# Performance work log

Measured on AMD Instinct MI355X. Metric: run time of the kernel, lower is better.

The kernel has to match this reference:

```python
import jax, jax.numpy as jnp
import numpy as np

# ---- dims (see shape_source) ----
N_NODES = 100_000
N_EDGES = 600_000
N_GRAPHS = 512
N_NODE_FEAT = 90   # atom-type vocabulary
H = 128            # n_hidden_feat
E_FEAT = 256       # n_edge_net_feat
G_FEAT = 128       # n_graph_feat
N_CONV = 3         # n_conv * n_edge_labels, conv_labels = [0,0,0]
SCALE = 0.05


def setup_inputs() -> dict:
    key = jax.random.key(0)
    ks = jax.random.split(key, 16)
    nodes = jax.random.randint(ks[0], (N_NODES,), 0, N_NODE_FEAT)
    edge_sources = jax.random.randint(ks[1], (N_EDGES,), 0, N_NODES)
    edge_targets = jax.random.randint(ks[2], (N_EDGES,), 0, N_NODES)
    graph_indices = jnp.sort(jax.random.randint(ks[3], (N_NODES,), 0, N_GRAPHS))
    node_counts = jnp.maximum(jnp.bincount(graph_indices, length=N_GRAPHS), 1).astype(jnp.float32)

    def rn(k, shape):
        return jax.random.normal(k, shape, jnp.float32) * SCALE

    return {
        "nodes": nodes,
        "edge_sources": edge_sources,
        "edge_targets": edge_targets,
        "graph_indices": graph_indices,
        "node_counts": node_counts,
        # learned parameters
        "embed": rn(ks[4], (N_NODE_FEAT, H)),           # NodeEmbedding table
        "Wg": rn(ks[5], (N_CONV, H, H)),                # gate linear per conv (bias=False)
        "We1": rn(ks[6], (N_CONV, H, E_FEAT)),          # EdgeNetwork layer 1 per conv
        "We2": rn(ks[7], (N_CONV, E_FEAT, H)),          # EdgeNetwork layer 2 per conv
        "Wp": rn(ks[8], (H, H)),                        # LinearPooling
        "Wfc1": rn(ks[9], (H, G_FEAT)), "bfc1": jnp.zeros((G_FEAT,), jnp.float32),
        "Wfc2": rn(ks[10], (G_FEAT, G_FEAT)), "bfc2": jnp.zeros((G_FEAT,), jnp.float32),
        "Wr": rn(ks[11], (G_FEAT, 1)), "br": jnp.zeros((1,), jnp.float32),
    }


def reference(nodes, edge_sources, edge_targets, graph_indices, node_counts,
              embed, Wg, We1, We2, Wp, Wfc1, bfc1, Wfc2, bfc2, Wr, br):
    sp = jax.nn.softplus
    # NodeEmbedding: atom-type lookup -> [N, H]
    x = embed[nodes]
    # Gated graph convolutions: gather -> edge MLP + gate -> scatter-add -> residual
    for i in range(N_CONV):
        z = x[edge_sources]                               # [E, H] gather
        e = sp(z @ We1[i]) @ We2[i]                       # EdgeNetwork (2 layers, no shortcut)
        m = jax.nn.sigmoid(z @ Wg[i]) * sp(e)             # gate * edge_activation(message)
        agg = jax.ops.segment_sum(m, edge_targets, num_segments=N_NODES)  # scatter-add
        x = x + sp(agg)                                   # node_activation + residual
    # LinearPooling (last conv only): per-graph mean of linear(x)
    y = jax.ops.segment_sum(x @ Wp, graph_indices, num_segments=N_GRAPHS) / node_counts[:, None]
    # GraphPooling with n_steps=1: activation only (no batch norm)
    g = sp(y)
    # FullConnection stack (n_fc=2)
    g = sp(g @ Wfc1 + bfc1)
    g = sp(g @ Wfc2 + bfc2)
    return g @ Wr + br
```

## Files before the change

kernel.cpp:

```cpp
#include <hip/hip_runtime.h>
#include <hip/hip_bf16.h>

typedef unsigned short u16;
typedef __attribute__((ext_vector_type(8))) short short8;
typedef __attribute__((ext_vector_type(4))) float f32x4;
typedef __attribute__((ext_vector_type(16))) float f32x16;
typedef __attribute__((ext_vector_type(2))) __bf16 bf16x2;

#define NNODES 100000
#define NEDGES 600000
#define NGRAPHS 512
#define HF 128
#define EF 256
#define GB 32
#define NTILES 3125
#define GRID_CONV 512

#define PLD 264
__device__ __forceinline__ int cidx(int chunk, int row){ return chunk * PLD + row * 8; }

__device__ __forceinline__ float bfu(u16 u){ return __uint_as_float(((unsigned)u) << 16); }
__device__ __forceinline__ u16 f2bf(float f){
    unsigned u = __float_as_uint(f);
    unsigned r = (u + 0x7fff + ((u >> 16) & 1)) >> 16;
    return (u16)r;
}
__device__ __forceinline__ unsigned pack2(float a, float b){
    bf16x2 v = { (__bf16)a, (__bf16)b };
    return __builtin_bit_cast(unsigned, v);
}

#if __has_builtin(__builtin_amdgcn_rcpf)
#define RCP1(x) __builtin_amdgcn_rcpf(x)
#else
#define RCP1(x) (1.f / (x))
#endif

__device__ __forceinline__ float sp_f(float x){
    return __logf(1.f + __expf(x));
}
__device__ __forceinline__ float sig_f(float x){
    return RCP1(1.f + __expf(-x));
}
__device__ __forceinline__ float lf(const void* p, long i, bool f32){
    return f32 ? ((const float*)p)[i] : bfu(((const u16*)p)[i]);
}

__device__ __forceinline__ bool is_f32(const void* probe){
    const u16* p = (const u16*)probe;
    int lane = threadIdx.x & 63;
    int c = 0;
#pragma unroll
    for (int i = 0; i < 4; i++) c += (fabsf(bfu(p[lane * 4 + i])) > 1.0f) ? 1 : 0;
#pragma unroll
    for (int off = 32; off; off >>= 1) c += __shfl_xor(c, off, 64);
    return c > 8;
}

__global__ __launch_bounds__(256) void prep_kernel(const void* __restrict__ wg,
                                                   const void* __restrict__ we1,
                                                   const void* __restrict__ we2,
                                                   const void* __restrict__ wp,
                                                   const void* __restrict__ wfc1,
                                                   const void* __restrict__ wfc2,
                                                   u16* __restrict__ pwg,
                                                   u16* __restrict__ pwe1,
                                                   u16* __restrict__ pwe2,
                                                   u16* __restrict__ pwp,
                                                   u16* __restrict__ pf1,
                                                   u16* __restrict__ pf2,
                                                   const void* __restrict__ emb,
                                                   const int* __restrict__ tgt,
                                                   int* __restrict__ counts,
                                                   float* __restrict__ xsum){
    int b = blockIdx.x, t = threadIdx.x;
    if (b < 960) {
        bool f32 = is_f32(emb);
        int i = b * 256 + t;
        int c = i / 81920, r = i % 81920;
        const void* src; u16* dst; int N, KN, l;
        if (r < 16384)      { src = wg;  dst = pwg;  N = HF; KN = 16384; l = r; }
        else if (r < 49152) { src = we1; dst = pwe1; N = EF; KN = 32768; l = r - 16384; }
        else                { src = we2; dst = pwe2; N = HF; KN = 32768; l = r - 49152; }
        int j = l & 7, lane = (l >> 3) & 63, rest = l >> 9;
        int NT = N >> 5;
        int nt = rest % NT, ks = rest / NT;
        int k = ks * 16 + (lane >> 5) * 8 + j;
        int n = nt * 32 + (lane & 31);
        long base = (long)c * KN;
        dst[base + l] = f2bf(lf(src, base + (long)k * N + n, f32));
    } else if (b < 1152) {
        bool f32 = is_f32(emb);
        int i = (b - 960) * 256 + t;
        int c = i / 16384, l = i % 16384;
        const void* src = (c == 0) ? wp : (c == 1) ? wfc1 : wfc2;
        u16* dst = (c == 0) ? pwp : (c == 1) ? pf1 : pf2;
        int j = l & 7, lane = (l >> 3) & 63, rest = l >> 9;
        int nt = rest & 7, kt = rest >> 3;
        int k = kt * 32 + (lane >> 4) * 8 + j;
        int n = nt * 16 + (lane & 15);
        dst[l] = f2bf(lf(src, (long)k * HF + n, f32));
    } else if (b < 3496) {
        int e = (b - 1152) * 256 + t;
        if (e < NEDGES) atomicAdd(&counts[tgt[e]], 1);
    } else {
        int i = (b - 3496) * 256 + t;
        ((float4*)xsum)[i] = make_float4(0.f, 0.f, 0.f, 0.f);
    }
}

__global__ __launch_bounds__(256) void scan1_kernel(const int* __restrict__ counts,
                                                    int* __restrict__ row_ptr,
                                                    int* __restrict__ bsums){
    __shared__ int s[256];
    int t = threadIdx.x;
    int i = blockIdx.x * 256 + t;
    int v = (i < NNODES) ? counts[i] : 0;
    s[t] = v; __syncthreads();
    for (int off = 1; off < 256; off <<= 1) {
        int a = (t >= off) ? s[t - off] : 0;
        __syncthreads();
        s[t] += a;
        __syncthreads();
    }
    if (i < NNODES) row_ptr[i] = s[t] - v;
    if (t == 255) bsums[blockIdx.x] = s[255];
}

__global__ __launch_bounds__(512) void scan2_kernel(const int* __restrict__ bsums,
                                                    int* __restrict__ boffs, int nb){
    __shared__ int s[512];
    int t = threadIdx.x;
    int v = (t < nb) ? bsums[t] : 0;
    s[t] = v; __syncthreads();
    for (int off = 1; off < 512; off <<= 1) {
        int a = (t >= off) ? s[t - off] : 0;
        __syncthreads();
        s[t] += a;
        __syncthreads();
    }
    if (t < nb) boffs[t] = s[t] - v;
}

__global__ __launch_bounds__(256) void scan3_kernel(int* __restrict__ row_ptr,
                                                    const int* __restrict__ boffs,
                                                    int* __restrict__ cursor){
    int i = blockIdx.x * 256 + threadIdx.x;
    if (i < NNODES) {
        int r = row_ptr[i] + boffs[blockIdx.x];
        row_ptr[i] = r;
        cursor[i]  = r;
    }
}

__global__ __launch_bounds__(256) void fill_kernel(const int* __restrict__ src,
                                                   const int* __restrict__ tgt,
                                                   int* __restrict__ cursor,
                                                   int* __restrict__ es){
    int e = blockIdx.x * 256 + threadIdx.x;
    if (e < NEDGES) {
        int pos = atomicAdd(&cursor[tgt[e]], 1);
        es[pos] = src[e];
    }
}

struct ConvW { short8 wu0[8], wu1[8], wc[16], wg[8]; };

__device__ __forceinline__ void load_w(ConvW& W, const u16* __restrict__ pwg,
                                       const u16* __restrict__ pwe1,
                                       const u16* __restrict__ pwe2,
                                       int w, int lane){
#pragma unroll
    for (int ks = 0; ks < 8; ks++) {
        W.wu0[ks] = *(const short8*)(pwe1 + (((ks * 8 + w) * 64 + lane) << 3));
        W.wu1[ks] = *(const short8*)(pwe1 + (((ks * 8 + w + 4) * 64 + lane) << 3));
        W.wg[ks]  = *(const short8*)(pwg  + (((ks * 4 + w) * 64 + lane) << 3));
    }
#pragma unroll
    for (int jj = 0; jj < 16; jj++)
        W.wc[jj] = *(const short8*)(pwe2 + (((jj * 4 + w) * 64 + lane) << 3));
}

__device__ __forceinline__ void conv_loop1(const ConvW& W, const u16* xs, u16* us,
                                           int w, int lane, f32x16& aG_out){
    const int half = lane >> 5, nn = lane & 31;
    f32x16 acc0 = {}, acc1 = {}, g = {};
#pragma unroll
    for (int ks = 0; ks < 8; ks++) {
        short8 B = *(const short8*)(&xs[cidx(ks * 2 + half, nn)]);
        acc0 = __builtin_amdgcn_mfma_f32_32x32x16_bf16(W.wu0[ks], B, acc0, 0, 0, 0);
        acc1 = __builtin_amdgcn_mfma_f32_32x32x16_bf16(W.wu1[ks], B, acc1, 0, 0, 0);
        g    = __builtin_amdgcn_mfma_f32_32x32x16_bf16(W.wg[ks],  B, g,    0, 0, 0);
    }
#pragma unroll
    for (int q = 0; q < 4; q++) {
        uint2 d;
        d.x = pack2(sp_f(acc0[q*4+0]), sp_f(acc0[q*4+1]));
        d.y = pack2(sp_f(acc0[q*4+2]), sp_f(acc0[q*4+3]));
        *(uint2*)(&us[cidx(w * 4 + q, nn) + half * 4]) = d;
        uint2 e;
        e.x = pack2(sp_f(acc1[q*4+0]), sp_f(acc1[q*4+1]));
        e.y = pack2(sp_f(acc1[q*4+2]), sp_f(acc1[q*4+3]));
        *(uint2*)(&us[cidx(16 + w * 4 + q, nn) + half * 4]) = e;
    }
    aG_out = g;
}

__device__ __forceinline__ void conv_loop2(const ConvW& W, const u16* us,
                                           const f32x16& aG, u16* __restrict__ M,
                                           long row0, int w, int lane){
    const int half = lane >> 5, nn = lane & 31;
    f32x16 aT = {};
#pragma unroll
    for (int jj = 0; jj < 16; jj++) {
        short8 B = *(const short8*)(&us[cidx(jj * 2 + half, nn)]);
        aT = __builtin_amdgcn_mfma_f32_32x32x16_bf16(W.wc[jj], B, aT, 0, 0, 0);
    }
    long node = row0 + nn;
#pragma unroll
    for (int q = 0; q < 4; q++) {
        int h0 = w * 32 + half * 4 + q * 8;
        uint2 d;
        d.x = pack2(sig_f(aG[q*4+0]) * sp_f(aT[q*4+0]),
                    sig_f(aG[q*4+1]) * sp_f(aT[q*4+1]));
        d.y = pack2(sig_f(aG[q*4+2]) * sp_f(aT[q*4+2]),
                    sig_f(aG[q*4+3]) * sp_f(aT[q*4+3]));
        *(uint2*)(M + node * HF + h0) = d;
    }
}

__global__ __launch_bounds__(256, 2) void conv0_mfma(const int* __restrict__ nodes,
                                                     const void* __restrict__ emb,
                                                     u16* __restrict__ x,
                                                     const u16* __restrict__ pwg,
                                                     const u16* __restrict__ pwe1,
                                                     const u16* __restrict__ pwe2,
                                                     u16* __restrict__ M){
    __shared__ u16 xs[16 * PLD];
    __shared__ u16 us[32 * PLD];
    const int t = threadIdx.x;
    const int w = t >> 6, lane = t & 63;
    const int r0 = t >> 4, q = t & 15;
    const bool f32 = is_f32(emb);

    ConvW W;
    load_w(W, pwg, pwe1, pwe2, w, lane);

    const float4* ef = (const float4*)emb;
    const uint4*  eu = (const uint4*)emb;
    uint4* xg = (uint4*)x;

    int tile = blockIdx.x;
    {
        long row0 = (long)tile * 32;
        int v0 = nodes[row0 + r0], v1 = nodes[row0 + r0 + 16];
        uint4 b0, b1;
        if (f32) {
            float4 f0 = ef[(long)v0 * 32 + q * 2], f1 = ef[(long)v0 * 32 + q * 2 + 1];
            float4 f2 = ef[(long)v1 * 32 + q * 2], f3 = ef[(long)v1 * 32 + q * 2 + 1];
            b0.x = pack2(f0.x, f0.y); b0.y = pack2(f0.z, f0.w);
            b0.z = pack2(f1.x, f1.y); b0.w = pack2(f1.z, f1.w);
            b1.x = pack2(f2.x, f2.y); b1.y = pack2(f2.z, f2.w);
            b1.z = pack2(f3.x, f3.y); b1.w = pack2(f3.z, f3.w);
        } else {
            b0 = eu[(long)v0 * 16 + q];
            b1 = eu[(long)v1 * 16 + q];
        }
        xg[(row0 + r0) * 16 + q] = b0;
        xg[(row0 + r0 + 16) * 16 + q] = b1;
        *(uint4*)(&xs[cidx(q, r0)]) = b0;
        *(uint4*)(&xs[cidx(q, r0 + 16)]) = b1;
    }
    __syncthreads();

    for (;;) {
        long row0 = (long)tile * 32;
        int nxt = tile + GRID_CONV;
        bool have = nxt < NTILES;
        uint4 nb0 = {}, nb1 = {};
        float4 nf0 = {}, nf1 = {}, nf2 = {}, nf3 = {};
        if (have) {
            long nr = (long)nxt * 32;
            int v0 = nodes[nr + r0], v1 = nodes[nr + r0 + 16];
            if (f32) {
                nf0 = ef[(long)v0 * 32 + q * 2]; nf1 = ef[(long)v0 * 32 + q * 2 + 1];
                nf2 = ef[(long)v1 * 32 + q * 2]; nf3 = ef[(long)v1 * 32 + q * 2 + 1];
            } else {
                nb0 = eu[(long)v0 * 16 + q];
                nb1 = eu[(long)v1 * 16 + q];
            }
        }
        f32x16 aG;
        conv_loop1(W, xs, us, w, lane, aG);
        __syncthreads();
        if (have) {
            uint4 b0 = nb0, b1 = nb1;
            if (f32) {
                b0.x = pack2(nf0.x, nf0.y); b0.y = pack2(nf0.z, nf0.w);
                b0.z = pack2(nf1.x, nf1.y); b0.w = pack2(nf1.z, nf1.w);
                b1.x = pack2(nf2.x, nf2.y); b1.y = pack2(nf2.z, nf2.w);
                b1.z = pack2(nf3.x, nf3.y); b1.w = pack2(nf3.z, nf3.w);
            }
            long nr = (long)nxt * 32;
            xg[(nr + r0) * 16 + q] = b0;
            xg[(nr + r0 + 16) * 16 + q] = b1;
            *(uint4*)(&xs[cidx(q, r0)]) = b0;
            *(uint4*)(&xs[cidx(q, r0 + 16)]) = b1;
        }
        conv_loop2(W, us, aG, M, row0, w, lane);
        if (!have) break;
        __syncthreads();
        tile = nxt;
    }
}

__global__ __launch_bounds__(256, 2) void conv_mfma(const u16* __restrict__ x,
                                                    const u16* __restrict__ pwg,
                                                    const u16* __restrict__ pwe1,
                                                    const u16* __restrict__ pwe2,
                                                    u16* __restrict__ M){
    __shared__ u16 xs[16 * PLD];
    __shared__ u16 us[32 * PLD];
    const int t = threadIdx.x;
    const int w = t >> 6, lane = t & 63;
    const int r0 = t >> 4, q = t & 15;

    ConvW W;
    load_w(W, pwg, pwe1, pwe2, w, lane);

    const uint4* xg = (const uint4*)x;
    int tile = blockIdx.x;
    {
        long row0 = (long)tile * 32;
        uint4 b0 = xg[(row0 + r0) * 16 + q];
        uint4 b1 = xg[(row0 + r0 + 16) * 16 + q];
        *(uint4*)(&xs[cidx(q, r0)]) = b0;
        *(uint4*)(&xs[cidx(q, r0 + 16)]) = b1;
    }
    __syncthreads();

    for (;;) {
        long row0 = (long)tile * 32;
        int nxt = tile + GRID_CONV;
        bool have = nxt < NTILES;
        uint4 nb0 = {}, nb1 = {};
        if (have) {
            long nr = (long)nxt * 32;
            nb0 = xg[(nr + r0) * 16 + q];
            nb1 = xg[(nr + r0 + 16) * 16 + q];
        }
        f32x16 aG;
        conv_loop1(W, xs, us, w, lane, aG);
        __syncthreads();
        if (have) {
            *(uint4*)(&xs[cidx(q, r0)]) = nb0;
            *(uint4*)(&xs[cidx(q, r0 + 16)]) = nb1;
        }
        conv_loop2(W, us, aG, M, row0, w, lane);
        if (!have) break;
        __syncthreads();
        tile = nxt;
    }
}

__global__ __launch_bounds__(256) void agg_kernel(const u16* __restrict__ M,
                                                  const int* __restrict__ row_ptr,
                                                  const int* __restrict__ counts,
                                                  const int* __restrict__ es,
                                                  u16* __restrict__ x){
    int wid = blockIdx.x * 4 + (threadIdx.x >> 6);
    int lane = threadIdx.x & 63;
    long v = (long)wid * 4 + (lane >> 4);
    int l = lane & 15;
    if (v >= NNODES) return;
    int start = row_ptr[v], cnt = counts[v];
    float a0=0.f,a1=0.f,a2=0.f,a3=0.f,a4=0.f,a5=0.f,a6=0.f,a7=0.f;
    float b0=0.f,b1=0.f,b2=0.f,b3=0.f,b4=0.f,b5=0.f,b6=0.f,b7=0.f;
    const uint4* Mu = (const uint4*)M;
    int e = 0;
    for (; e + 3 < cnt; e += 4) {
        int s0 = es[start + e],     s1 = es[start + e + 1];
        int s2 = es[start + e + 2], s3 = es[start + e + 3];
        uint4 u0 = Mu[(long)s0 * 16 + l];
        uint4 u1 = Mu[(long)s1 * 16 + l];
        uint4 u2 = Mu[(long)s2 * 16 + l];
        uint4 u3 = Mu[(long)s3 * 16 + l];
        a0 += bfu((u16)u0.x); a1 += bfu((u16)(u0.x >> 16));
        a2 += bfu((u16)u0.y); a3 += bfu((u16)(u0.y >> 16));
        a4 += bfu((u16)u0.z); a5 += bfu((u16)(u0.z >> 16));
        a6 += bfu((u16)u0.w); a7 += bfu((u16)(u0.w >> 16));
        b0 += bfu((u16)u1.x); b1 += bfu((u16)(u1.x >> 16));
        b2 += bfu((u16)u1.y); b3 += bfu((u16)(u1.y >> 16));
        b4 += bfu((u16)u1.z); b5 += bfu((u16)(u1.z >> 16));
        b6 += bfu((u16)u1.w); b7 += bfu((u16)(u1.w >> 16));
        a0 += bfu((u16)u2.x); a1 += bfu((u16)(u2.x >> 16));
        a2 += bfu((u16)u2.y); a3 += bfu((u16)(u2.y >> 16));
        a4 += bfu((u16)u2.z); a5 += bfu((u16)(u2.z >> 16));
        a6 += bfu((u16)u2.w); a7 += bfu((u16)(u2.w >> 16));
        b0 += bfu((u16)u3.x); b1 += bfu((u16)(u3.x >> 16));
        b2 += bfu((u16)u3.y); b3 += bfu((u16)(u3.y >> 16));
        b4 += bfu((u16)u3.z); b5 += bfu((u16)(u3.z >> 16));
        b6 += bfu((u16)u3.w); b7 += bfu((u16)(u3.w >> 16));
    }
    for (; e < cnt; e++) {
        int s0 = es[start + e];
        uint4 u0 = Mu[(long)s0 * 16 + l];
        a0 += bfu((u16)u0.x); a1 += bfu((u16)(u0.x >> 16));
        a2 += bfu((u16)u0.y); a3 += bfu((u16)(u0.y >> 16));
        a4 += bfu((u16)u0.z); a5 += bfu((u16)(u0.z >> 16));
        a6 += bfu((u16)u0.w); a7 += bfu((u16)(u0.w >> 16));
    }
    a0 += b0; a1 += b1; a2 += b2; a3 += b3;
    a4 += b4; a5 += b5; a6 += b6; a7 += b7;
    uint4* xu = (uint4*)x;
    uint4 xv = xu[v * 16 + l];
    xv.x = pack2(bfu((u16)xv.x) + sp_f(a0), bfu((u16)(xv.x >> 16)) + sp_f(a1));
    xv.y = pack2(bfu((u16)xv.y) + sp_f(a2), bfu((u16)(xv.y >> 16)) + sp_f(a3));
    xv.z = pack2(bfu((u16)xv.z) + sp_f(a4), bfu((u16)(xv.z >> 16)) + sp_f(a5));
    xv.w = pack2(bfu((u16)xv.w) + sp_f(a6), bfu((u16)(xv.w >> 16)) + sp_f(a7));
    xu[v * 16 + l] = xv;
}

__global__ __launch_bounds__(256) void pool_kernel(const u16* __restrict__ x,
                                                   const int* __restrict__ gidx,
                                                   float* __restrict__ xsum){
    int wave = blockIdx.x * 4 + (threadIdx.x >> 6);
    int lane = threadIdx.x & 63;
    long base = (long)wave * 64;
    if (base >= NNODES) return;
    long end = base + 64; if (end > NNODES) end = NNODES;
    const unsigned* xu = (const unsigned*)x;
    int gcur = gidx[base];
    float a0 = 0.f, a1 = 0.f;
    for (long v = base; v < end; v++) {
        int g = gidx[v];
        if (g != gcur) {
            atomicAdd(&xsum[gcur * HF + lane * 2 + 0], a0);
            atomicAdd(&xsum[gcur * HF + lane * 2 + 1], a1);
            a0 = a1 = 0.f; gcur = g;
        }
        unsigned u = xu[v * 64 + lane];
        a0 += bfu((u16)u);
        a1 += bfu((u16)(u >> 16));
    }
    atomicAdd(&xsum[gcur * HF + lane * 2 + 0], a0);
    atomicAdd(&xsum[gcur * HF + lane * 2 + 1], a1);
}

__global__ __launch_bounds__(256) void head_mfma(const float* __restrict__ xsum,
                                                 const void* __restrict__ ncnt,
                                                 const u16* __restrict__ pwp,
                                                 const u16* __restrict__ pf1,
                                                 const u16* __restrict__ pf2,
                                                 const void* __restrict__ bfc1,
                                                 const void* __restrict__ bfc2,
                                                 const void* __restrict__ Wr,
                                                 const void* __restrict__ br,
                                                 void* __restrict__ out,
                                                 const void* __restrict__ probe){
    __shared__ u16 hibuf[2][GB][136];
    __shared__ u16 lobuf[2][GB][136];
    const int t = threadIdx.x;
    const int w = t >> 6, lane = t & 63;
    const int quad = lane >> 4, nr = lane & 15;
    const bool f32 = is_f32(probe);
    const int g0 = blockIdx.x * GB;

    for (int i = t; i < GB * 64; i += 256) {
        int g = i >> 6, c = (i & 63) * 2;
        float f0 = xsum[(g0 + g) * HF + c], f1 = xsum[(g0 + g) * HF + c + 1];
        u16 h0 = f2bf(f0), h1 = f2bf(f1);
        *(unsigned*)&hibuf[0][g][c] = (unsigned)h0 | ((unsigned)h1 << 16);
        *(unsigned*)&lobuf[0][g][c] = pack2(f0 - bfu(h0), f1 - bfu(h1));
    }
    __syncthreads();

    float rc[2];
#pragma unroll
    for (int nt = 0; nt < 2; nt++) rc[nt] = RCP1(lf(ncnt, g0 + nt * 16 + nr, f32));

    int cur = 0;
    for (int layer = 0; layer < 3; layer++) {
        const u16* pw = (layer == 0) ? pwp : (layer == 1) ? pf1 : pf2;
        const void* bias = (layer == 1) ? bfc1 : bfc2;
        int nxt = cur ^ 1;
#pragma unroll
        for (int c = 0; c < 2; c++) {
            int et = w * 2 + c;
            short8 A[4];
#pragma unroll
            for (int kt = 0; kt < 4; kt++)
                A[kt] = *(const short8*)(pw + (((kt * 8 + et) * 64 + lane) << 3));
#pragma unroll
            for (int nt = 0; nt < 2; nt++) {
                f32x4 acc = {0.f, 0.f, 0.f, 0.f};
#pragma unroll
                for (int kt = 0; kt < 4; kt++) {
                    short8 bh = *(const short8*)(&hibuf[cur][nt * 16 + nr][kt * 32 + quad * 8]);
                    short8 bl = *(const short8*)(&lobuf[cur][nt * 16 + nr][kt * 32 + quad * 8]);
                    acc = __builtin_amdgcn_mfma_f32_16x16x32_bf16(A[kt], bh, acc, 0, 0, 0);
                    acc = __builtin_amdgcn_mfma_f32_16x16x32_bf16(A[kt], bl, acc, 0, 0, 0);
                }
                int feat0 = et * 16 + quad * 4;
                float f[4];
#pragma unroll
                for (int r = 0; r < 4; r++) {
                    float a = (layer == 0) ? acc[r] * rc[nt]
                                           : acc[r] + lf(bias, feat0 + r, f32);
                    f[r] = sp_f(a);
                }
                u16 h[4]; float lo[4];
#pragma unroll
                for (int r = 0; r < 4; r++) { h[r] = f2bf(f[r]); lo[r] = f[r] - bfu(h[r]); }
                uint2 dh, dl;
                dh.x = (unsigned)h[0] | ((unsigned)h[1] << 16);
                dh.y = (unsigned)h[2] | ((unsigned)h[3] << 16);
                dl.x = pack2(lo[0], lo[1]);
                dl.y = pack2(lo[2], lo[3]);
                *(uint2*)&hibuf[nxt][nt * 16 + nr][feat0] = dh;
                *(uint2*)&lobuf[nxt][nt * 16 + nr][feat0] = dl;
            }
        }
        __syncthreads();
        cur = nxt;
    }

    int g = t >> 3, sub = t & 7;
    float p = 0.f;
    for (int k = sub * 16; k < sub * 16 + 16; k++) {
        float v = bfu(hibuf[cur][g][k]) + bfu(lobuf[cur][g][k]);
        p += v * lf(Wr, k, f32);
    }
    p += __shfl_down(p, 4, 64);
    p += __shfl_down(p, 2, 64);
    p += __shfl_down(p, 1, 64);
    if (sub == 0) {
        float res = p + lf(br, 0, f32);
        if (f32) ((float*)out)[g0 + g] = res;
        else     ((u16*)out)[g0 + g]  = f2bf(res);
    }
}

extern "C" void kernel_launch(void* const* d_in, const int* in_sizes, int n_in,
                              void* d_out, int out_size, void* d_ws, size_t ws_size,
                              hipStream_t stream) {
    const int* nodes = (const int*)d_in[0];
    const int* esrc  = (const int*)d_in[1];
    const int* etgt  = (const int*)d_in[2];
    const int* gidx  = (const int*)d_in[3];

    size_t off = 0;
    char* w = (char*)d_ws;
    auto take = [&](size_t bytes) -> void* {
        void* p = w + off;
        off = (off + bytes + 255) & ~(size_t)255;
        return p;
    };

    u16* pwg     = (u16*)take((size_t)3 * HF * HF * 2);
    u16* pwe1    = (u16*)take((size_t)3 * HF * EF * 2);
    u16* pwe2    = (u16*)take((size_t)3 * EF * HF * 2);
    u16* pwp     = (u16*)take((size_t)HF * HF * 2);
    u16* pf1     = (u16*)take((size_t)HF * HF * 2);
    u16* pf2     = (u16*)take((size_t)HF * HF * 2);
    int* counts  = (int*)take((size_t)NNODES * 4);
    int* row_ptr = (int*)take((size_t)NNODES * 4);
    int* cursor  = (int*)take((size_t)NNODES * 4);
    int* es      = (int*)take((size_t)NEDGES * 4);
    int* bsums   = (int*)take(2048);
    int* boffs   = (int*)take(2048);
    float* xsum  = (float*)take((size_t)NGRAPHS * HF * 4);
    u16* x       = (u16*)take((size_t)NNODES * HF * 2);
    u16* M       = (u16*)take((size_t)NNODES * HF * 2);

    hipMemsetAsync(counts, 0, (size_t)NNODES * 4, stream);

    prep_kernel<<<3560, 256, 0, stream>>>(d_in[6], d_in[7], d_in[8],
                                          d_in[9], d_in[10], d_in[12],
                                          pwg, pwe1, pwe2, pwp, pf1, pf2,
                                          d_in[5], etgt, counts, xsum);

    const int NB_SCAN = (NNODES + 255) / 256;
    const int NB_EDGE = (NEDGES + 255) / 256;
    scan1_kernel<<<NB_SCAN, 256, 0, stream>>>(counts, row_ptr, bsums);
    scan2_kernel<<<1, 512, 0, stream>>>(bsums, boffs, NB_SCAN);
    scan3_kernel<<<NB_SCAN, 256, 0, stream>>>(row_ptr, boffs, cursor);
    fill_kernel<<<NB_EDGE, 256, 0, stream>>>(esrc, etgt, cursor, es);

    const int NBA = (NNODES + 15) / 16;
    conv0_mfma<<<GRID_CONV, 256, 0, stream>>>(nodes, d_in[5], x, pwg, pwe1, pwe2, M);
    agg_kernel<<<NBA, 256, 0, stream>>>(M, row_ptr, counts, es, x);
    conv_mfma<<<GRID_CONV, 256, 0, stream>>>(x,
        pwg + (size_t)1 * HF * HF, pwe1 + (size_t)1 * HF * EF, pwe2 + (size_t)1 * EF * HF, M);
    agg_kernel<<<NBA, 256, 0, stream>>>(M, row_ptr, counts, es, x);
    conv_mfma<<<GRID_CONV, 256, 0, stream>>>(x,
        pwg + (size_t)2 * HF * HF, pwe1 + (size_t)2 * HF * EF, pwe2 + (size_t)2 * EF * HF, M);
    agg_kernel<<<NBA, 256, 0, stream>>>(M, row_ptr, counts, es, x);

    pool_kernel<<<(NNODES + 255) / 256, 256, 0, stream>>>(x, gidx, xsum);
    head_mfma<<<NGRAPHS / GB, 256, 0, stream>>>(xsum, d_in[4], pwp, pf1, pf2,
                                                d_in[11], d_in[13], d_in[14], d_in[15],
                                                d_out, d_in[5]);
}
```

Measured before the change: 388.0 us.

## Stage edge-network weights in LDS instead of registers, halve conv grid

Moves the EdgeNetwork weight fragments (We1, We2) out of per-thread registers into a large dynamic LDS buffer (about 153 KB per block), and reads the gate weights directly from global memory in each tile. The conv grid drops from 512 to 256 blocks, since only one block per CU fits with that LDS footprint. The aim is to free VGPRs and avoid per-wave redundant weight registers. In exchange every MFMA now needs extra LDS and global loads, and occupancy is limited to one block per CU.

```diff
diff --git a/kernel.cpp b/kernel.cpp
--- a/kernel.cpp
+++ b/kernel.cpp
@@ -14,10 +14,12 @@
 #define EF 256
 #define GB 32
 #define NTILES 3125
-#define GRID_CONV 512
+#define CONV_GRID 256
 
 #define PLD 264
 __device__ __forceinline__ int cidx(int chunk, int row){ return chunk * PLD + row * 8; }
+
+#define SMEM_BYTES 156416
 
 __device__ __forceinline__ float bfu(u16 u){ return __uint_as_float(((unsigned)u) << 16); }
 __device__ __forceinline__ u16 f2bf(float f){
@@ -164,58 +166,57 @@
     }
 }
 
-struct ConvW { short8 wu0[8], wu1[8], wc[16], wg[8]; };
-
-__device__ __forceinline__ void load_w(ConvW& W, const u16* __restrict__ pwg,
-                                       const u16* __restrict__ pwe1,
-                                       const u16* __restrict__ pwe2,
-                                       int w, int lane){
-#pragma unroll
-    for (int ks = 0; ks < 8; ks++) {
-        W.wu0[ks] = *(const short8*)(pwe1 + (((ks * 8 + w) * 64 + lane) << 3));
-        W.wu1[ks] = *(const short8*)(pwe1 + (((ks * 8 + w + 4) * 64 + lane) << 3));
-        W.wg[ks]  = *(const short8*)(pwg  + (((ks * 4 + w) * 64 + lane) << 3));
-    }
-#pragma unroll
-    for (int jj = 0; jj < 16; jj++)
-        W.wc[jj] = *(const short8*)(pwe2 + (((jj * 4 + w) * 64 + lane) << 3));
-}
-
-__device__ __forceinline__ void conv_loop1(const ConvW& W, const u16* xs, u16* us,
-                                           int w, int lane, f32x16& aG_out){
+__device__ __forceinline__ void conv_tile(const u16* w1, const u16* w2,
+                                          const u16* xs, u16* us,
+                                          const u16* __restrict__ pwg,
+                                          f32x16& aG_out, f32x16& aT_out,
+                                          int w, int lane, int phase){
     const int half = lane >> 5, nn = lane & 31;
-    f32x16 acc0 = {}, acc1 = {}, g = {};
-#pragma unroll
-    for (int ks = 0; ks < 8; ks++) {
-        short8 B = *(const short8*)(&xs[cidx(ks * 2 + half, nn)]);
-        acc0 = __builtin_amdgcn_mfma_f32_32x32x16_bf16(W.wu0[ks], B, acc0, 0, 0, 0);
-        acc1 = __builtin_amdgcn_mfma_f32_32x32x16_bf16(W.wu1[ks], B, acc1, 0, 0, 0);
-        g    = __builtin_amdgcn_mfma_f32_32x32x16_bf16(W.wg[ks],  B, g,    0, 0, 0);
-    }
-#pragma unroll
-    for (int q = 0; q < 4; q++) {
-        uint2 d;
-        d.x = pack2(sp_f(acc0[q*4+0]), sp_f(acc0[q*4+1]));
-        d.y = pack2(sp_f(acc0[q*4+2]), sp_f(acc0[q*4+3]));
-        *(uint2*)(&us[cidx(w * 4 + q, nn) + half * 4]) = d;
-        uint2 e;
-        e.x = pack2(sp_f(acc1[q*4+0]), sp_f(acc1[q*4+1]));
-        e.y = pack2(sp_f(acc1[q*4+2]), sp_f(acc1[q*4+3]));
-        *(uint2*)(&us[cidx(16 + w * 4 + q, nn) + half * 4]) = e;
-    }
-    aG_out = g;
-}
-
-__device__ __forceinline__ void conv_loop2(const ConvW& W, const u16* us,
-                                           const f32x16& aG, u16* __restrict__ M,
-                                           long row0, int w, int lane){
+    if (phase == 0) {
+        f32x16 acc0 = {}, acc1 = {};
+#pragma unroll
+        for (int ks = 0; ks < 8; ks++) {
+            short8 A0 = *(const short8*)(w1 + (((ks * 8 + w) * 64 + lane) << 3));
+            short8 A1 = *(const short8*)(w1 + (((ks * 8 + w + 4) * 64 + lane) << 3));
+            short8 B  = *(const short8*)(&xs[cidx(ks * 2 + half, nn)]);
+            acc0 = __builtin_amdgcn_mfma_f32_32x32x16_bf16(A0, B, acc0, 0, 0, 0);
+            acc1 = __builtin_amdgcn_mfma_f32_32x32x16_bf16(A1, B, acc1, 0, 0, 0);
+        }
+#pragma unroll
+        for (int q = 0; q < 4; q++) {
+            uint2 d;
+            d.x = pack2(sp_f(acc0[q*4+0]), sp_f(acc0[q*4+1]));
+            d.y = pack2(sp_f(acc0[q*4+2]), sp_f(acc0[q*4+3]));
+            *(uint2*)(&us[cidx(w * 4 + q, nn) + half * 4]) = d;
+            uint2 e;
+            e.x = pack2(sp_f(acc1[q*4+0]), sp_f(acc1[q*4+1]));
+            e.y = pack2(sp_f(acc1[q*4+2]), sp_f(acc1[q*4+3]));
+            *(uint2*)(&us[cidx(16 + w * 4 + q, nn) + half * 4]) = e;
+        }
+        f32x16 aG = {};
+#pragma unroll
+        for (int ks = 0; ks < 8; ks++) {
+            short8 A = *(const short8*)(pwg + (((ks * 4 + w) * 64 + lane) << 3));
+            short8 B = *(const short8*)(&xs[cidx(ks * 2 + half, nn)]);
+            aG = __builtin_amdgcn_mfma_f32_32x32x16_bf16(A, B, aG, 0, 0, 0);
+        }
+        aG_out = aG;
+    } else {
+        f32x16 aT = {};
+#pragma unroll
+        for (int jj = 0; jj < 16; jj++) {
+            short8 A = *(const short8*)(w2 + (((jj * 4 + w) * 64 + lane) << 3));
+            short8 B = *(const short8*)(&us[cidx(jj * 2 + half, nn)]);
+            aT = __builtin_amdgcn_mfma_f32_32x32x16_bf16(A, B, aT, 0, 0, 0);
+        }
+        aT_out = aT;
+    }
+}
+
+__device__ __forceinline__ void conv_write(const f32x16& aG, const f32x16& aT,
+                                           u16* __restrict__ M, long row0,
+                                           int w, int lane){
     const int half = lane >> 5, nn = lane & 31;
-    f32x16 aT = {};
-#pragma unroll
-    for (int jj = 0; jj < 16; jj++) {
-        short8 B = *(const short8*)(&us[cidx(jj * 2 + half, nn)]);
-        aT = __builtin_amdgcn_mfma_f32_32x32x16_bf16(W.wc[jj], B, aT, 0, 0, 0);
-    }
     long node = row0 + nn;
 #pragma unroll
     for (int q = 0; q < 4; q++) {
@@ -229,22 +230,25 @@
     }
 }
 
-__global__ __launch_bounds__(256, 2) void conv0_mfma(const int* __restrict__ nodes,
-                                                     const void* __restrict__ emb,
-                                                     u16* __restrict__ x,
-                                                     const u16* __restrict__ pwg,
-                                                     const u16* __restrict__ pwe1,
-                                                     const u16* __restrict__ pwe2,
-                                                     u16* __restrict__ M){
-    __shared__ u16 xs[16 * PLD];
-    __shared__ u16 us[32 * PLD];
+__global__ __launch_bounds__(256) void conv0_mfma(const int* __restrict__ nodes,
+                                                  const void* __restrict__ emb,
+                                                  u16* __restrict__ x,
+                                                  const u16* __restrict__ pwg,
+                                                  const u16* __restrict__ pwe1,
+                                                  const u16* __restrict__ pwe2,
+                                                  u16* __restrict__ M){
+    extern __shared__ u16 smem[];
+    u16* w1 = smem;
+    u16* w2 = smem + 32768;
+    u16* xs = smem + 65536;
+    u16* us = xs + 16 * PLD;
     const int t = threadIdx.x;
     const int w = t >> 6, lane = t & 63;
     const int r0 = t >> 4, q = t & 15;
     const bool f32 = is_f32(emb);
 
-    ConvW W;
-    load_w(W, pwg, pwe1, pwe2, w, lane);
+    for (int i = t; i < 4096; i += 256) ((uint4*)w1)[i] = ((const uint4*)pwe1)[i];
+    for (int i = t; i < 4096; i += 256) ((uint4*)w2)[i] = ((const uint4*)pwe2)[i];
 
     const float4* ef = (const float4*)emb;
     const uint4*  eu = (const uint4*)emb;
@@ -275,7 +279,7 @@
 
     for (;;) {
         long row0 = (long)tile * 32;
-        int nxt = tile + GRID_CONV;
+        int nxt = tile + CONV_GRID;
         bool have = nxt < NTILES;
         uint4 nb0 = {}, nb1 = {};
         float4 nf0 = {}, nf1 = {}, nf2 = {}, nf3 = {};
@@ -290,8 +294,8 @@
                 nb1 = eu[(long)v1 * 16 + q];
             }
         }
-        f32x16 aG;
-        conv_loop1(W, xs, us, w, lane, aG);
+        f32x16 aG, aT;
+        conv_tile(w1, w2, xs, us, pwg, aG, aT, w, lane, 0);
         __syncthreads();
         if (have) {
             uint4 b0 = nb0, b1 = nb1;
@@ -307,26 +311,30 @@
             *(uint4*)(&xs[cidx(q, r0)]) = b0;
             *(uint4*)(&xs[cidx(q, r0 + 16)]) = b1;
         }
-        conv_loop2(W, us, aG, M, row0, w, lane);
+        conv_tile(w1, w2, xs, us, pwg, aG, aT, w, lane, 1);
+        conv_write(aG, aT, M, row0, w, lane);
         if (!have) break;
         __syncthreads();
         tile = nxt;
     }
 }
 
-__global__ __launch_bounds__(256, 2) void conv_mfma(const u16* __restrict__ x,
-                                                    const u16* __restrict__ pwg,
-                                                    const u16* __restrict__ pwe1,
-                                                    const u16* __restrict__ pwe2,
-                                                    u16* __restrict__ M){
-    __shared__ u16 xs[16 * PLD];
-    __shared__ u16 us[32 * PLD];
+__global__ __launch_bounds__(256) void conv_mfma(const u16* __restrict__ x,
+                                                 const u16* __restrict__ pwg,
+                                                 const u16* __restrict__ pwe1,
+                                                 const u16* __restrict__ pwe2,
+                                                 u16* __restrict__ M){
+    extern __shared__ u16 smem[];
+    u16* w1 = smem;
+    u16* w2 = smem + 32768;
+    u16* xs = smem + 65536;
+    u16* us = xs + 16 * PLD;
     const int t = threadIdx.x;
     const int w = t >> 6, lane = t & 63;
     const int r0 = t >> 4, q = t & 15;
 
-    ConvW W;
-    load_w(W, pwg, pwe1, pwe2, w, lane);
+    for (int i = t; i < 4096; i += 256) ((uint4*)w1)[i] = ((const uint4*)pwe1)[i];
+    for (int i = t; i < 4096; i += 256) ((uint4*)w2)[i] = ((const uint4*)pwe2)[i];
 
     const uint4* xg = (const uint4*)x;
     int tile = blockIdx.x;
@@ -341,7 +349,7 @@
 
     for (;;) {
         long row0 = (long)tile * 32;
-        int nxt = tile + GRID_CONV;
+        int nxt = tile + CONV_GRID;
         bool have = nxt < NTILES;
         uint4 nb0 = {}, nb1 = {};
         if (have) {
@@ -349,14 +357,15 @@
             nb0 = xg[(nr + r0) * 16 + q];
             nb1 = xg[(nr + r0 + 16) * 16 + q];
         }
-        f32x16 aG;
-        conv_loop1(W, xs, us, w, lane, aG);
+        f32x16 aG, aT;
+        conv_tile(w1, w2, xs, us, pwg, aG, aT, w, lane, 0);
         __syncthreads();
         if (have) {
             *(uint4*)(&xs[cidx(q, r0)]) = nb0;
             *(uint4*)(&xs[cidx(q, r0 + 16)]) = nb1;
         }
-        conv_loop2(W, us, aG, M, row0, w, lane);
+        conv_tile(w1, w2, xs, us, pwg, aG, aT, w, lane, 1);
+        conv_write(aG, aT, M, row0, w, lane);
         if (!have) break;
         __syncthreads();
         tile = nxt;
@@ -573,6 +582,11 @@
     u16* x       = (u16*)take((size_t)NNODES * HF * 2);
     u16* M       = (u16*)take((size_t)NNODES * HF * 2);
 
+    hipFuncSetAttribute((const void*)conv0_mfma,
+                        hipFuncAttributeMaxDynamicSharedMemorySize, SMEM_BYTES);
+    hipFuncSetAttribute((const void*)conv_mfma,
+                        hipFuncAttributeMaxDynamicSharedMemorySize, SMEM_BYTES);
+
     hipMemsetAsync(counts, 0, (size_t)NNODES * 4, stream);
 
     prep_kernel<<<3560, 256, 0, stream>>>(d_in[6], d_in[7], d_in[8],
@@ -588,12 +602,13 @@
     fill_kernel<<<NB_EDGE, 256, 0, stream>>>(esrc, etgt, cursor, es);
 
     const int NBA = (NNODES + 15) / 16;
-    conv0_mfma<<<GRID_CONV, 256, 0, stream>>>(nodes, d_in[5], x, pwg, pwe1, pwe2, M);
+    conv0_mfma<<<CONV_GRID, 256, SMEM_BYTES, stream>>>(nodes, d_in[5], x,
+                                                       pwg, pwe1, pwe2, M);
     agg_kernel<<<NBA, 256, 0, stream>>>(M, row_ptr, counts, es, x);
-    conv_mfma<<<GRID_CONV, 256, 0, stream>>>(x,
+    conv_mfma<<<CONV_GRID, 256, SMEM_BYTES, stream>>>(x,
         pwg + (size_t)1 * HF * HF, pwe1 + (size_t)1 * HF * EF, pwe2 + (size_t)1 * EF * HF, M);
     agg_kernel<<<NBA, 256, 0, stream>>>(M, row_ptr, counts, es, x);
-    conv_mfma<<<GRID_CONV, 256, 0, stream>>>(x,
+    conv_mfma<<<CONV_GRID, 256, SMEM_BYTES, stream>>>(x,
         pwg + (size_t)2 * HF * HF, pwe1 + (size_t)2 * HF * EF, pwe2 + (size_t)2 * EF * HF, M);
     agg_kernel<<<NBA, 256, 0, stream>>>(M, row_ptr, counts, es, x);
 
```

After: 443.5 us. 1.14x slower.
